# Kernel tuning notes

Measured on AMD Instinct MI355X. Metric: run time of the kernel, lower is better.

The kernel has to match this reference:

```python
import jax, jax.numpy as jnp
import numpy as np

ALPHA = 0.2  # LeakyReLU negative slope
NEG_INF = -9e15

def setup_inputs() -> dict:
    key = jax.random.key(0)
    k1, k2, k3, k4 = jax.random.split(key, 4)
    N, IN_F, OUT_F = 12288, 256, 128
    h = jax.random.normal(k1, (N, IN_F), dtype=jnp.float32)
    adj = jax.random.randint(k2, (N, N), 0, 2, dtype=jnp.int32)
    # Xavier-uniform-like init with gain 1.414
    limW = 1.414 * np.sqrt(6.0 / (IN_F + OUT_F))
    W = jax.random.uniform(k3, (IN_F, OUT_F), dtype=jnp.float32, minval=-limW, maxval=limW)
    lima = 1.414 * np.sqrt(6.0 / (2 * OUT_F + 1))
    a = jax.random.uniform(k4, (2 * OUT_F, 1), dtype=jnp.float32, minval=-lima, maxval=lima)
    return {"h": h, "adj": adj, "W": W, "a": a}

def reference(h, adj, W, a):
    out_f = W.shape[1]
    Wh = h @ W                      # [N, out_f]
    Wh1 = Wh @ a[:out_f, :]         # [N, 1]
    Wh2 = Wh @ a[out_f:, :]         # [N, 1]
    e = Wh1 + Wh2.T                 # [N, N] broadcast-add scores
    e = jnp.where(e > 0, e, ALPHA * e)  # LeakyReLU
    scores = jnp.where(adj > 0, e, NEG_INF)
    attention = jax.nn.softmax(scores, axis=1)  # dropout is identity at inference
    h_prime = attention @ Wh        # [N, out_f]
    return jax.nn.elu(h_prime)      # concat=True -> ELU
```

## Files before the change

### kernel.cpp

```cpp
#include <hip/hip_runtime.h>

#define NN   12288
#define FIN  256
#define FOUT 128
#define ALPHA 0.2f

typedef __attribute__((ext_vector_type(8))) _Float16 half8v;
typedef __attribute__((ext_vector_type(4))) float float4v;
typedef __attribute__((ext_vector_type(4))) int   int4v;


__global__ __launch_bounds__(128) void k_wh(
    const float* __restrict__ h,
    const float* __restrict__ W,
    const float* __restrict__ a,
    _Float16* __restrict__ WhT2,
    float* __restrict__ Wh1, float* __restrict__ Wh2)
{
    __shared__ __align__(16) float hs[16 * FIN];
    __shared__ float sP1[2][16], sP2[2][16];
    const int t = threadIdx.x;
    const int row0 = blockIdx.x * 16;

    const float4v* hsrc = (const float4v*)(h + (size_t)row0 * FIN);
    float4v* hdst = (float4v*)hs;
    #pragma unroll
    for (int i = 0; i < 8; ++i) hdst[t + i * 128] = hsrc[t + i * 128];
    __syncthreads();

    float acc[16];
    #pragma unroll
    for (int r = 0; r < 16; ++r) acc[r] = 0.f;

    for (int k = 0; k < FIN; k += 4) {
        const float w0 = W[(k + 0) * FOUT + t];
        const float w1 = W[(k + 1) * FOUT + t];
        const float w2 = W[(k + 2) * FOUT + t];
        const float w3 = W[(k + 3) * FOUT + t];
        #pragma unroll
        for (int r = 0; r < 16; ++r) {
            const float4v hv = *(const float4v*)&hs[r * FIN + k];
            float s = acc[r];
            s = fmaf(hv.x, w0, s);
            s = fmaf(hv.y, w1, s);
            s = fmaf(hv.z, w2, s);
            s = fmaf(hv.w, w3, s);
            acc[r] = s;
        }
    }

    half8v pk0, pk1;
    #pragma unroll
    for (int r = 0; r < 8; ++r)  pk0[r] = (_Float16)acc[r];
    #pragma unroll
    for (int r = 0; r < 8; ++r)  pk1[r] = (_Float16)acc[8 + r];
    _Float16* dst = WhT2 + (size_t)(row0 >> 5) * 4096 + t * 32 + (row0 & 16);
    *(half8v*)(dst)     = pk0;
    *(half8v*)(dst + 8) = pk1;

    const float a1t = a[t];
    const float a2t = a[FOUT + t];
    const int lane = t & 63, wv = t >> 6;
    #pragma unroll
    for (int r = 0; r < 16; ++r) {
        float v1 = acc[r] * a1t;
        float v2 = acc[r] * a2t;
        #pragma unroll
        for (int off = 1; off < 64; off <<= 1) {
            v1 += __shfl_xor(v1, off, 64);
            v2 += __shfl_xor(v2, off, 64);
        }
        if (lane == 0) { sP1[wv][r] = v1; sP2[wv][r] = v2; }
    }
    __syncthreads();
    if (t < 16) {
        Wh1[row0 + t] = sP1[0][t] + sP1[1][t];
        Wh2[row0 + t] = sP2[0][t] + sP2[1][t];
    }
}

__global__ __launch_bounds__(256) void k_max(
    const float* __restrict__ Wh2, float* __restrict__ outmax)
{
    __shared__ float sm[4];
    float m = -1e30f;
    for (int i = threadIdx.x; i < NN; i += 256) m = fmaxf(m, Wh2[i]);
    #pragma unroll
    for (int off = 1; off < 64; off <<= 1) m = fmaxf(m, __shfl_xor(m, off, 64));
    if ((threadIdx.x & 63) == 0) sm[threadIdx.x >> 6] = m;
    __syncthreads();
    if (threadIdx.x == 0)
        outmax[0] = fmaxf(fmaxf(sm[0], sm[1]), fmaxf(sm[2], sm[3]));
}

__global__ __launch_bounds__(256, 3) void k_attn(
    const int* __restrict__ adj,
    const _Float16* __restrict__ WhT2,
    const float* __restrict__ Wh1, const float* __restrict__ Wh2,
    const float* __restrict__ maxp,
    float* __restrict__ pC, float* __restrict__ pS)
{
    __shared__ __align__(16) _Float16 tile[2][128 * 32];
    const int tid  = threadIdx.x;
    const int w    = tid >> 6;
    const int lane = tid & 63;
    const int m    = lane & 15;
    const int q    = lane >> 4;
    const int rowbase = blockIdx.x * 128 + w * 32;
    const int J    = gridDim.y;
    const int jy   = blockIdx.y;
    const int jlen = NN / J;
    const int jbeg = jy * jlen;
    const int iters = jlen / 32;

    const float mxv  = maxp[0];
    const float wh1a = Wh1[rowbase + m];
    const float wh1b = Wh1[rowbase + 16 + m];
    const float tma = wh1a + mxv; const float Ma = fmaxf(tma, ALPHA * tma);
    const float tmb = wh1b + mxv; const float Mb = fmaxf(tmb, ALPHA * tmb);

    const int* rowA = adj + (size_t)(rowbase + m) * NN;
    const int* rowB = adj + (size_t)(rowbase + 16 + m) * NN;

    float4v c[2][8];
    #pragma unroll
    for (int rg = 0; rg < 2; ++rg)
        #pragma unroll
        for (int t = 0; t < 8; ++t) c[rg][t] = (float4v){0.f, 0.f, 0.f, 0.f};
    float Sa = 0.f, Sb = 0.f;

    {
        const float4v* src = (const float4v*)(WhT2 + (size_t)(jbeg >> 5) * 4096);
        float4v* dst = (float4v*)&tile[0][0];
        dst[tid * 2 + 0] = src[tid * 2 + 0];
        dst[tid * 2 + 1] = src[tid * 2 + 1];
    }
    __syncthreads();

    int buf = 0;
    for (int it = 0; it < iters; ++it) {
        const int j0 = jbeg + it * 32;
        const int jb = j0 + q * 8;
        const bool pre = (it + 1 < iters);
        float4v s0, s1;
        if (pre) {
            const float4v* src = (const float4v*)(WhT2 + (size_t)((j0 + 32) >> 5) * 4096);
            s0 = src[tid * 2 + 0];
            s1 = src[tid * 2 + 1];
        }

        const int4v aa0 = *(const int4v*)(rowA + jb);
        const int4v aa1 = *(const int4v*)(rowA + jb + 4);
        const int4v ab0 = *(const int4v*)(rowB + jb);
        const int4v ab1 = *(const int4v*)(rowB + jb + 4);
        const float4v w0 = *(const float4v*)(Wh2 + jb);
        const float4v w1 = *(const float4v*)(Wh2 + jb + 4);
        const float wv[8] = {w0.x, w0.y, w0.z, w0.w, w1.x, w1.y, w1.z, w1.w};
        const int   ava[8] = {aa0.x, aa0.y, aa0.z, aa0.w, aa1.x, aa1.y, aa1.z, aa1.w};
        const int   avb[8] = {ab0.x, ab0.y, ab0.z, ab0.w, ab1.x, ab1.y, ab1.z, ab1.w};

        half8v afa, afb;
        #pragma unroll
        for (int jj = 0; jj < 8; ++jj) {
            float e = wh1a + wv[jj]; e = fmaxf(e, ALPHA * e);
            const float p = ava[jj] ? __expf(e - Ma) : 0.f;
            const _Float16 ph = (_Float16)p;
            afa[jj] = ph; Sa += (float)ph;
        }
        #pragma unroll
        for (int jj = 0; jj < 8; ++jj) {
            float e = wh1b + wv[jj]; e = fmaxf(e, ALPHA * e);
            const float p = avb[jj] ? __expf(e - Mb) : 0.f;
            const _Float16 ph = (_Float16)p;
            afb[jj] = ph; Sb += (float)ph;
        }

        half8v bfr[8];
        #pragma unroll
        for (int t = 0; t < 8; ++t)
            bfr[t] = *(const half8v*)&tile[buf][(t * 16 + m) * 32 + q * 8];

        #pragma unroll
        for (int t = 0; t < 8; ++t) {
            c[0][t] = __builtin_amdgcn_mfma_f32_16x16x32_f16(afa, bfr[t], c[0][t], 0, 0, 0);
            c[1][t] = __builtin_amdgcn_mfma_f32_16x16x32_f16(afb, bfr[t], c[1][t], 0, 0, 0);
        }

        if (pre) {
            float4v* dst = (float4v*)&tile[buf ^ 1][0];
            dst[tid * 2 + 0] = s0;
            dst[tid * 2 + 1] = s1;
        }
        __syncthreads();
        buf ^= 1;
    }

    Sa += __shfl_xor(Sa, 16, 64); Sa += __shfl_xor(Sa, 32, 64);
    Sb += __shfl_xor(Sb, 16, 64); Sb += __shfl_xor(Sb, 32, 64);
    if (q == 0) {
        pS[(size_t)jy * NN + rowbase + m]      = Sa;
        pS[(size_t)jy * NN + rowbase + 16 + m] = Sb;
    }
    #pragma unroll
    for (int rg = 0; rg < 2; ++rg)
        #pragma unroll
        for (int t = 0; t < 8; ++t)
            #pragma unroll
            for (int reg = 0; reg < 4; ++reg) {
                const int row = rowbase + rg * 16 + q * 4 + reg;
                pC[((size_t)jy * NN + row) * FOUT + t * 16 + m] = c[rg][t][reg];
            }
}

__global__ __launch_bounds__(256) void k_reduce(
    const float* __restrict__ pC, const float* __restrict__ pS,
    float* __restrict__ out, int J)
{
    const int idx = blockIdx.x * 256 + threadIdx.x;
    const int row = idx >> 5;
    const int c4  = (idx & 31) * 4;
    float4v acc = (float4v){0.f, 0.f, 0.f, 0.f};
    float S = 0.f;
    for (int j = 0; j < J; ++j) {
        const float4v v = *(const float4v*)(pC + ((size_t)j * NN + row) * FOUT + c4);
        acc.x += v.x; acc.y += v.y; acc.z += v.z; acc.w += v.w;
        S += pS[(size_t)j * NN + row];
    }
    const float inv = 1.f / fmaxf(S, 1e-30f);
    float4v r;
    #pragma unroll
    for (int k = 0; k < 4; ++k) {
        const float v = acc[k] * inv;
        r[k] = (v > 0.f) ? v : (__expf(v) - 1.f);
    }
    *(float4v*)(out + (size_t)row * FOUT + c4) = r;
}

__global__ __launch_bounds__(256) void k_attn_fb(
    const int* __restrict__ adj,
    const _Float16* __restrict__ WhT2,
    const float* __restrict__ Wh1, const float* __restrict__ Wh2,
    const float* __restrict__ maxp,
    float* __restrict__ out)
{
    __shared__ __align__(16) float cbuf[4][8][64][4];
    __shared__ float sbuf[4][16];
    const int tid  = threadIdx.x;
    const int w    = tid >> 6;
    const int lane = tid & 63;
    const int m    = lane & 15;
    const int q    = lane >> 4;
    const int i    = blockIdx.x * 16 + m;

    const float wh1 = Wh1[i];
    const float tm = wh1 + maxp[0];
    const float Mi = fmaxf(tm, ALPHA * tm);

    float4v c[8];
    #pragma unroll
    for (int t = 0; t < 8; ++t) c[t] = (float4v){0.f, 0.f, 0.f, 0.f};
    float S = 0.f;
    const int* adjrow = adj + (size_t)i * NN;

    for (int j0 = w * (NN / 4); j0 < (w + 1) * (NN / 4); j0 += 32) {
        const int jb = j0 + q * 8;
        const int4v  a0 = *(const int4v*)(adjrow + jb);
        const int4v  a1 = *(const int4v*)(adjrow + jb + 4);
        const float4v w0 = *(const float4v*)(Wh2 + jb);
        const float4v w1 = *(const float4v*)(Wh2 + jb + 4);
        half8v bfr[8];
        #pragma unroll
        for (int t = 0; t < 8; ++t)
            bfr[t] = *(const half8v*)(WhT2 + (size_t)(j0 >> 5) * 4096 + (t * 16 + m) * 32 + q * 8);
        const float wvv[8] = {w0.x, w0.y, w0.z, w0.w, w1.x, w1.y, w1.z, w1.w};
        const int av[8] = {a0.x, a0.y, a0.z, a0.w, a1.x, a1.y, a1.z, a1.w};
        half8v af;
        #pragma unroll
        for (int jj = 0; jj < 8; ++jj) {
            float e = wh1 + wvv[jj]; e = fmaxf(e, ALPHA * e);
            const float p = av[jj] ? __expf(e - Mi) : 0.f;
            const _Float16 ph = (_Float16)p;
            af[jj] = ph; S += (float)ph;
        }
        #pragma unroll
        for (int t = 0; t < 8; ++t)
            c[t] = __builtin_amdgcn_mfma_f32_16x16x32_f16(af, bfr[t], c[t], 0, 0, 0);
    }
    S += __shfl_xor(S, 16, 64);
    S += __shfl_xor(S, 32, 64);
    if (lane < 16) sbuf[w][lane] = S;
    #pragma unroll
    for (int t = 0; t < 8; ++t) *(float4v*)&cbuf[w][t][lane][0] = c[t];
    __syncthreads();
    #pragma unroll
    for (int tt = 0; tt < 2; ++tt) {
        const int t = w * 2 + tt;
        float4v cs = *(const float4v*)&cbuf[0][t][lane][0];
        #pragma unroll
        for (int w2 = 1; w2 < 4; ++w2) {
            const float4v o = *(const float4v*)&cbuf[w2][t][lane][0];
            cs.x += o.x; cs.y += o.y; cs.z += o.z; cs.w += o.w;
        }
        #pragma unroll
        for (int reg = 0; reg < 4; ++reg) {
            const int mloc = q * 4 + reg;
            const float Sr = sbuf[0][mloc] + sbuf[1][mloc] + sbuf[2][mloc] + sbuf[3][mloc];
            const float v = cs[reg] / fmaxf(Sr, 1e-30f);
            out[(size_t)(blockIdx.x * 16 + mloc) * FOUT + t * 16 + m] =
                (v > 0.f) ? v : (__expf(v) - 1.f);
        }
    }
}

extern "C" void kernel_launch(void* const* d_in, const int* in_sizes, int n_in,
                              void* d_out, int out_size, void* d_ws, size_t ws_size,
                              hipStream_t stream) {
    const float* h   = (const float*)d_in[0];
    const int*   adj = (const int*)d_in[1];
    const float* W   = (const float*)d_in[2];
    const float* a   = (const float*)d_in[3];
    float* out = (float*)d_out;

    char* ws = (char*)d_ws;
    float* Wh1 = (float*)ws;
    float* Wh2 = (float*)(ws + 49152);
    float* mx  = (float*)(ws + 98304);
    _Float16* WhT2 = (_Float16*)(ws + 98560);
    const size_t base_need = 98560ULL + 3145728ULL;

    int J = 8;
    while (J > 1 &&
           base_need + (size_t)J * NN * 4 + (size_t)J * NN * FOUT * 4 > ws_size)
        J >>= 1;
    const bool ok =
        base_need + (size_t)NN * 4 + (size_t)NN * FOUT * 4 <= ws_size;

    k_wh  <<<NN / 16, 128, 0, stream>>>(h, W, a, WhT2, Wh1, Wh2);
    k_max <<<1, 256, 0, stream>>>(Wh2, mx);
    if (ok) {
        float* pS = (float*)(ws + base_need);
        float* pC = pS + (size_t)J * NN;
        k_attn<<<dim3(NN / 128, J), 256, 0, stream>>>(adj, WhT2, Wh1, Wh2, mx, pC, pS);
        k_reduce<<<(NN * (FOUT / 4)) / 256, 256, 0, stream>>>(pC, pS, out, J);
    } else {
        k_attn_fb<<<NN / 16, 256, 0, stream>>>(adj, WhT2, Wh1, Wh2, mx, out);
    }
}
```

Baseline: 897.6 us.

## Use direct global-to-LDS loads and process 64 columns per attention iteration

The attention kernel now stages WhT2 tiles with global_load_lds straight into shared memory instead of through registers. Each iteration handles 64 neighbour columns (two 32-wide subtiles), which halves the number of barriers and deepens the memory-level parallelism. The adjacency rows are read with nontemporal loads to avoid polluting cache. The row sum now accumulates the fp32 probability rather than the fp16-rounded value, which slightly changes normalisation numerics, and the larger unroll may raise register pressure under the 3-blocks-per-SM launch bound.

After: 880.9 us. Within noise of the previous version (-1.9%).

```diff
diff --git a/kernel.cpp b/kernel.cpp
--- a/kernel.cpp
+++ b/kernel.cpp
@@ -9,6 +9,11 @@
 typedef __attribute__((ext_vector_type(4))) float float4v;
 typedef __attribute__((ext_vector_type(4))) int   int4v;
 
+
+#define GLL16(gp, lp)                                                          \
+    __builtin_amdgcn_global_load_lds(                                          \
+        (const __attribute__((address_space(1))) void*)(gp),                   \
+        (__attribute__((address_space(3))) void*)(lp), 16, 0, 0)
 
 __global__ __launch_bounds__(128) void k_wh(
     const float* __restrict__ h,
@@ -93,6 +98,23 @@
         outmax[0] = fmaxf(fmaxf(sm[0], sm[1]), fmaxf(sm[2], sm[3]));
 }
 
+static __device__ __forceinline__ half8v build_p(
+    const int4v a0, const int4v a1, const float* wvv,
+    const float wh1, const float M, float& S)
+{
+    const int av[8] = {a0.x, a0.y, a0.z, a0.w, a1.x, a1.y, a1.z, a1.w};
+    half8v af;
+    #pragma unroll
+    for (int jj = 0; jj < 8; ++jj) {
+        float e = wh1 + wvv[jj];
+        e = fmaxf(e, ALPHA * e);
+        const float p = av[jj] ? __expf(e - M) : 0.f;
+        af[jj] = (_Float16)p;
+        S += p;
+    }
+    return af;
+}
+
 __global__ __launch_bounds__(256, 3) void k_attn(
     const int* __restrict__ adj,
     const _Float16* __restrict__ WhT2,
@@ -100,7 +122,7 @@
     const float* __restrict__ maxp,
     float* __restrict__ pC, float* __restrict__ pS)
 {
-    __shared__ __align__(16) _Float16 tile[2][128 * 32];
+    __shared__ __align__(16) _Float16 tile[2][2][4096];
     const int tid  = threadIdx.x;
     const int w    = tid >> 6;
     const int lane = tid & 63;
@@ -111,7 +133,7 @@
     const int jy   = blockIdx.y;
     const int jlen = NN / J;
     const int jbeg = jy * jlen;
-    const int iters = jlen / 32;
+    const int iters = jlen / 64;
 
     const float mxv  = maxp[0];
     const float wh1a = Wh1[rowbase + m];
@@ -130,67 +152,62 @@
     float Sa = 0.f, Sb = 0.f;
 
     {
-        const float4v* src = (const float4v*)(WhT2 + (size_t)(jbeg >> 5) * 4096);
-        float4v* dst = (float4v*)&tile[0][0];
-        dst[tid * 2 + 0] = src[tid * 2 + 0];
-        dst[tid * 2 + 1] = src[tid * 2 + 1];
+        const float4v* grp = (const float4v*)(WhT2 + (size_t)(jbeg >> 5) * 4096);
+        float4v* lb = (float4v*)&tile[0][0][0];
+        #pragma unroll
+        for (int k = 0; k < 4; ++k)
+            GLL16(grp + (w * 4 + k) * 64 + lane, lb + (w * 4 + k) * 64);
     }
     __syncthreads();
 
     int buf = 0;
     for (int it = 0; it < iters; ++it) {
-        const int j0 = jbeg + it * 32;
-        const int jb = j0 + q * 8;
-        const bool pre = (it + 1 < iters);
-        float4v s0, s1;
-        if (pre) {
-            const float4v* src = (const float4v*)(WhT2 + (size_t)((j0 + 32) >> 5) * 4096);
-            s0 = src[tid * 2 + 0];
-            s1 = src[tid * 2 + 1];
-        }
-
-        const int4v aa0 = *(const int4v*)(rowA + jb);
-        const int4v aa1 = *(const int4v*)(rowA + jb + 4);
-        const int4v ab0 = *(const int4v*)(rowB + jb);
-        const int4v ab1 = *(const int4v*)(rowB + jb + 4);
-        const float4v w0 = *(const float4v*)(Wh2 + jb);
-        const float4v w1 = *(const float4v*)(Wh2 + jb + 4);
-        const float wv[8] = {w0.x, w0.y, w0.z, w0.w, w1.x, w1.y, w1.z, w1.w};
-        const int   ava[8] = {aa0.x, aa0.y, aa0.z, aa0.w, aa1.x, aa1.y, aa1.z, aa1.w};
-        const int   avb[8] = {ab0.x, ab0.y, ab0.z, ab0.w, ab1.x, ab1.y, ab1.z, ab1.w};
-
-        half8v afa, afb;
-        #pragma unroll
-        for (int jj = 0; jj < 8; ++jj) {
-            float e = wh1a + wv[jj]; e = fmaxf(e, ALPHA * e);
-            const float p = ava[jj] ? __expf(e - Ma) : 0.f;
-            const _Float16 ph = (_Float16)p;
-            afa[jj] = ph; Sa += (float)ph;
-        }
-        #pragma unroll
-        for (int jj = 0; jj < 8; ++jj) {
-            float e = wh1b + wv[jj]; e = fmaxf(e, ALPHA * e);
-            const float p = avb[jj] ? __expf(e - Mb) : 0.f;
-            const _Float16 ph = (_Float16)p;
-            afb[jj] = ph; Sb += (float)ph;
-        }
-
-        half8v bfr[8];
-        #pragma unroll
-        for (int t = 0; t < 8; ++t)
-            bfr[t] = *(const half8v*)&tile[buf][(t * 16 + m) * 32 + q * 8];
+        const int j0 = jbeg + it * 64;
+
+        if (it + 1 < iters) {
+            const float4v* grp =
+                (const float4v*)(WhT2 + (size_t)((j0 + 64) >> 5) * 4096);
+            float4v* lb = (float4v*)&tile[buf ^ 1][0][0];
+            #pragma unroll
+            for (int k = 0; k < 4; ++k)
+                GLL16(grp + (w * 4 + k) * 64 + lane, lb + (w * 4 + k) * 64);
+        }
+
+        const int jb0 = j0 + q * 8;
+        const int jb1 = j0 + 32 + q * 8;
+        const int4v aA0 = __builtin_nontemporal_load((const int4v*)(rowA + jb0));
+        const int4v aA1 = __builtin_nontemporal_load((const int4v*)(rowA + jb0 + 4));
+        const int4v aA2 = __builtin_nontemporal_load((const int4v*)(rowA + jb1));
+        const int4v aA3 = __builtin_nontemporal_load((const int4v*)(rowA + jb1 + 4));
+        const int4v aB0 = __builtin_nontemporal_load((const int4v*)(rowB + jb0));
+        const int4v aB1 = __builtin_nontemporal_load((const int4v*)(rowB + jb0 + 4));
+        const int4v aB2 = __builtin_nontemporal_load((const int4v*)(rowB + jb1));
+        const int4v aB3 = __builtin_nontemporal_load((const int4v*)(rowB + jb1 + 4));
+        const float4v w00 = *(const float4v*)(Wh2 + jb0);
+        const float4v w01 = *(const float4v*)(Wh2 + jb0 + 4);
+        const float4v w10 = *(const float4v*)(Wh2 + jb1);
+        const float4v w11 = *(const float4v*)(Wh2 + jb1 + 4);
+        const float wv0[8] = {w00.x, w00.y, w00.z, w00.w, w01.x, w01.y, w01.z, w01.w};
+        const float wv1[8] = {w10.x, w10.y, w10.z, w10.w, w11.x, w11.y, w11.z, w11.w};
+
+        const half8v afa0 = build_p(aA0, aA1, wv0, wh1a, Ma, Sa);
+        const half8v afa1 = build_p(aA2, aA3, wv1, wh1a, Ma, Sa);
+        const half8v afb0 = build_p(aB0, aB1, wv0, wh1b, Mb, Sb);
+        const half8v afb1 = build_p(aB2, aB3, wv1, wh1b, Mb, Sb);
 
         #pragma unroll
         for (int t = 0; t < 8; ++t) {
-            c[0][t] = __builtin_amdgcn_mfma_f32_16x16x32_f16(afa, bfr[t], c[0][t], 0, 0, 0);
-            c[1][t] = __builtin_amdgcn_mfma_f32_16x16x32_f16(afb, bfr[t], c[1][t], 0, 0, 0);
-        }
-
-        if (pre) {
-            float4v* dst = (float4v*)&tile[buf ^ 1][0];
-            dst[tid * 2 + 0] = s0;
-            dst[tid * 2 + 1] = s1;
-        }
+            const half8v b = *(const half8v*)&tile[buf][0][(t * 16 + m) * 32 + q * 8];
+            c[0][t] = __builtin_amdgcn_mfma_f32_16x16x32_f16(afa0, b, c[0][t], 0, 0, 0);
+            c[1][t] = __builtin_amdgcn_mfma_f32_16x16x32_f16(afb0, b, c[1][t], 0, 0, 0);
+        }
+        #pragma unroll
+        for (int t = 0; t < 8; ++t) {
+            const half8v b = *(const half8v*)&tile[buf][1][(t * 16 + m) * 32 + q * 8];
+            c[0][t] = __builtin_amdgcn_mfma_f32_16x16x32_f16(afa1, b, c[0][t], 0, 0, 0);
+            c[1][t] = __builtin_amdgcn_mfma_f32_16x16x32_f16(afb1, b, c[1][t], 0, 0, 0);
+        }
+
         __syncthreads();
         buf ^= 1;
     }
@@ -273,15 +290,7 @@
         for (int t = 0; t < 8; ++t)
             bfr[t] = *(const half8v*)(WhT2 + (size_t)(j0 >> 5) * 4096 + (t * 16 + m) * 32 + q * 8);
         const float wvv[8] = {w0.x, w0.y, w0.z, w0.w, w1.x, w1.y, w1.z, w1.w};
-        const int av[8] = {a0.x, a0.y, a0.z, a0.w, a1.x, a1.y, a1.z, a1.w};
-        half8v af;
-        #pragma unroll
-        for (int jj = 0; jj < 8; ++jj) {
-            float e = wh1 + wvv[jj]; e = fmaxf(e, ALPHA * e);
-            const float p = av[jj] ? __expf(e - Mi) : 0.f;
-            const _Float16 ph = (_Float16)p;
-            af[jj] = ph; S += (float)ph;
-        }
+        const half8v af = build_p(a0, a1, wvv, wh1, Mi, S);
         #pragma unroll
         for (int t = 0; t < 8; ++t)
             c[t] = __builtin_amdgcn_mfma_f32_16x16x32_f16(af, bfr[t], c[t], 0, 0, 0);
```
